# Kernel optimization log

Hardware: AMD Instinct MI355X
Metric: run time of the kernel (lower is better)

Reference implementation:

```python
import jax, jax.numpy as jnp
import numpy as np

BLOCK = 32          # MX block size (group_size)
E4M3_MAX = 448.0    # max finite value of float8_e4m3fn
E4M3_EMAX = 8       # max exponent of e4m3 (used for shared-exponent offset per MX spec)
TINY = 1e-38        # guard for log2(0)


def _quant_e4m3(v):
    """Fake-quantize v to the float8_e4m3fn grid with rint (round-half-even)."""
    a = jnp.abs(v)
    # exponent of each element, clamped to [min_normal_exp=-6, emax=8]
    e = jnp.clip(jnp.floor(jnp.log2(jnp.maximum(a, TINY))), -6.0, 8.0)
    step = jnp.exp2(e - 3.0)  # 3 mantissa bits
    q = jnp.clip(jnp.round(a / step) * step, 0.0, E4M3_MAX)
    return jnp.sign(v) * q


def mx_quant(v):
    """npu_dynamic_mx_quant(axis=-1, block_size=32, dst=e4m3, round=rint).
    Returns (q_blocks [..., K//32, 32], e8m0 scale [..., K//32])."""
    K = v.shape[-1]
    vb = v.reshape(*v.shape[:-1], K // BLOCK, BLOCK)
    amax = jnp.max(jnp.abs(vb), axis=-1)
    # shared exponent: floor(log2(amax)) - emax_elem, as an e8m0 power-of-two scale
    se = jnp.where(amax > 0,
                   jnp.floor(jnp.log2(jnp.maximum(amax, TINY))) - E4M3_EMAX,
                   0.0)
    scale = jnp.exp2(jnp.clip(se, -127.0, 127.0))
    q = _quant_e4m3(vb / scale[..., None])
    return q, scale


def setup_inputs() -> dict:
    key = jax.random.key(0)
    k1, k2, k3 = jax.random.split(key, 3)
    B, S, K, N = 2, 2048, 4096, 4096
    x = jax.random.normal(k1, (B, S, K), dtype=jnp.float32)
    weight = jax.random.normal(k2, (N, K), dtype=jnp.float32) * 0.02  # Linear weight [out, in]
    bias = jax.random.normal(k3, (N,), dtype=jnp.float32) * 0.01
    return {"x": x, "weight": weight, "bias": bias}


def reference(x, weight, bias):
    ori_shape = x.shape
    x2 = x.reshape(-1, ori_shape[-1])            # [M, K]
    # weight quantized once at init in the original module; same math here
    qw, sw = mx_quant(weight)                    # [N, K/32, 32], [N, K/32]
    qx, sx = mx_quant(x2)                        # [M, K/32, 32], [M, K/32]
    # group-scaled dequant-matmul: per-block scale product applied per group
    dqx = qx * sx[..., None]
    dqw = qw * sw[..., None]
    out = jnp.einsum('mgb,ngb->mn', dqx, dqw) + bias
    return out.reshape(*ori_shape[:-1], -1)
```

## Files before the change

kernel.cpp:

```cpp
#include <hip/hip_runtime.h>
#include <hip/hip_bf16.h>
#include <stdint.h>

typedef __attribute__((ext_vector_type(8)))  __bf16 bf16x8;
typedef __attribute__((ext_vector_type(16))) float  floatx16;
typedef unsigned short ushort8 __attribute__((ext_vector_type(8)));

__device__ __forceinline__ uint16_t f32_to_bf16_rn(float f) {
    uint32_t u = __float_as_uint(f);
    uint32_t r = u + 0x7FFFu + ((u >> 16) & 1u);
    return (uint16_t)(r >> 16);
}

__global__ __launch_bounds__(256) void quant_dq2_kernel(
    const float* __restrict__ x, const float* __restrict__ w,
    uint16_t* __restrict__ dqx, uint16_t* __restrict__ dqw,
    int nxh, int ntoth)
{
    int t = blockIdx.x * blockDim.x + threadIdx.x;
    if (t >= ntoth) return;
    const float* src; uint16_t* dst; int idx;
    if (t < nxh) { src = x; dst = dqx; idx = t; }
    else         { src = w; dst = dqw; idx = t - nxh; }

    const float4* p = (const float4*)src + (size_t)idx * 4;
    float4 v0 = p[0], v1 = p[1], v2 = p[2], v3 = p[3];
    float r[16] = {v0.x, v0.y, v0.z, v0.w, v1.x, v1.y, v1.z, v1.w,
                   v2.x, v2.y, v2.z, v2.w, v3.x, v3.y, v3.z, v3.w};

    float am = 0.0f;
#pragma unroll
    for (int i = 0; i < 16; ++i) am = fmaxf(am, fabsf(r[i]));
    am = fmaxf(am, __shfl_xor(am, 1));

    float scale, iscale;
    if (am > 0.0f) {
        int se = (int)((__float_as_uint(am) >> 23) & 0xFF) - 135;
        se = se < -127 ? -127 : se;
        scale  = __uint_as_float((uint32_t)(se + 127) << 23);
        iscale = __uint_as_float((uint32_t)(127 - se) << 23);
    } else {
        scale = 1.0f; iscale = 1.0f;
    }

    uint16_t o[16];
#pragma unroll
    for (int i = 0; i < 16; ++i) {
        float sv = r[i] * iscale;
        float a  = fabsf(sv);
        int e = (int)((__float_as_uint(a) >> 23) & 0xFF) - 127;
        e = e < -6 ? -6 : (e > 8 ? 8 : e);
        float step  = __uint_as_float((uint32_t)(e - 3 + 127) << 23);
        float rstep = __uint_as_float((uint32_t)(3 - e + 127) << 23);
        float q = rintf(a * rstep) * step;
        q = fminf(q, 448.0f);
        float dq = copysignf(q, sv) * scale;
        o[i] = f32_to_bf16_rn(dq);
    }
    ushort8 lo, hi;
#pragma unroll
    for (int i = 0; i < 8; ++i) { lo[i] = o[i]; hi[i] = o[i + 8]; }
    ((ushort8*)dst)[idx * 2]     = lo;
    ((ushort8*)dst)[idx * 2 + 1] = hi;
}

#define BM 128
#define BN 128
#define BK 64

__global__ __launch_bounds__(256) void gemm_bt_bias(
    const uint16_t* __restrict__ A, const uint16_t* __restrict__ B,
    const float* __restrict__ bias, float* __restrict__ C,
    int M, int N, int K)
{
    __shared__ uint16_t sA[BM * BK];
    __shared__ uint16_t sB[BN * BK];

    const int tid  = threadIdx.x;
    const int wave = tid >> 6;
    const int lane = tid & 63;

    const int bm = blockIdx.y * BM;
    const int bn = blockIdx.x * BN;

    const int srow8  = lane >> 3;
    const int schunk = (lane & 7) ^ srow8;
    const int wrow   = wave * 32;

    const uint16_t* Ag = A + (size_t)(bm + wrow + srow8) * K + schunk * 8;
    const uint16_t* Bg = B + (size_t)(bn + wrow + srow8) * K + schunk * 8;

    const int wm  = (wave & 1) * 64;
    const int wn  = (wave >> 1) * 64;
    const int m32 = lane & 31;
    const int h   = lane >> 5;
    const int swz = m32 & 7;

    floatx16 acc[2][2];
#pragma unroll
    for (int i = 0; i < 2; ++i)
#pragma unroll
        for (int j = 0; j < 2; ++j)
#pragma unroll
            for (int r = 0; r < 16; ++r) acc[i][j][r] = 0.0f;

    for (int k0 = 0; k0 < K; k0 += BK) {
        __syncthreads();
#pragma unroll
        for (int c = 0; c < 4; ++c) {
            __builtin_amdgcn_global_load_lds(
                (const __attribute__((address_space(1))) void*)(Ag + (size_t)c * 8 * K + k0),
                (__attribute__((address_space(3))) void*)(sA + (wrow + c * 8) * BK),
                16, 0, 0);
        }
#pragma unroll
        for (int c = 0; c < 4; ++c) {
            __builtin_amdgcn_global_load_lds(
                (const __attribute__((address_space(1))) void*)(Bg + (size_t)c * 8 * K + k0),
                (__attribute__((address_space(3))) void*)(sB + (wrow + c * 8) * BK),
                16, 0, 0);
        }
        __syncthreads();

#pragma unroll
        for (int kk = 0; kk < 4; ++kk) {
            const int chunk = kk * 2 + h;
            const int slot  = chunk ^ swz;
            bf16x8 a0 = *(const bf16x8*)(sA + (wm      + m32) * BK + slot * 8);
            bf16x8 a1 = *(const bf16x8*)(sA + (wm + 32 + m32) * BK + slot * 8);
            bf16x8 b0 = *(const bf16x8*)(sB + (wn      + m32) * BK + slot * 8);
            bf16x8 b1 = *(const bf16x8*)(sB + (wn + 32 + m32) * BK + slot * 8);
            acc[0][0] = __builtin_amdgcn_mfma_f32_32x32x16_bf16(a0, b0, acc[0][0], 0, 0, 0);
            acc[0][1] = __builtin_amdgcn_mfma_f32_32x32x16_bf16(a0, b1, acc[0][1], 0, 0, 0);
            acc[1][0] = __builtin_amdgcn_mfma_f32_32x32x16_bf16(a1, b0, acc[1][0], 0, 0, 0);
            acc[1][1] = __builtin_amdgcn_mfma_f32_32x32x16_bf16(a1, b1, acc[1][1], 0, 0, 0);
        }
    }

#pragma unroll
    for (int j = 0; j < 2; ++j) {
        const int col = bn + wn + j * 32 + m32;
        const float bz = bias[col];
#pragma unroll
        for (int i = 0; i < 2; ++i) {
            const int rbase = bm + wm + i * 32 + 4 * h;
#pragma unroll
            for (int r = 0; r < 16; ++r) {
                const int row = rbase + (r & 3) + 8 * (r >> 2);
                C[(size_t)row * N + col] = acc[i][j][r] + bz;
            }
        }
    }
}

extern "C" void kernel_launch(void* const* d_in, const int* in_sizes, int n_in,
                              void* d_out, int out_size, void* d_ws, size_t ws_size,
                              hipStream_t stream) {
    const float* x    = (const float*)d_in[0];
    const float* w    = (const float*)d_in[1];
    const float* bias = (const float*)d_in[2];
    float* out = (float*)d_out;

    const int N = in_sizes[2];
    const int K = in_sizes[1] / N;
    const int M = in_sizes[0] / K;

    uint16_t* dqx = (uint16_t*)d_ws;
    uint16_t* dqw = dqx + (size_t)M * K;

    const int nxh   = (M * K) / 16;
    const int ntoth = nxh + (N * K) / 16;
    quant_dq2_kernel<<<(ntoth + 255) / 256, 256, 0, stream>>>(x, w, dqx, dqw, nxh, ntoth);

    dim3 grid(N / BN, M / BM);
    gemm_bt_bias<<<grid, 256, 0, stream>>>(dqx, dqw, bias, out, M, N, K);
}
```

Before: 320.3 us.

## Use 256x256 tiles with double-buffered LDS pipeline and XCD-aware block remap

Enlarges the GEMM workgroup tile to 256x256 with 512 threads and moves operands into 128KB of dynamic LDS split into two buffers. The next K-tile is prefetched while MFMAs run on the current one, using vmcnt waits and raw barriers in place of __syncthreads. Block IDs are remapped across the 8 XCDs for L2 locality, and B fragments are preloaded in registers while s_setprio is raised around the MFMA groups. This aims to cut global-load stalls and raise arithmetic intensity, at the cost of more registers and LDS, which limits occupancy. The grid also shrinks to 256 workgroups on the 256-CU part, leaving no second wave of blocks to hide stalls.

```diff
diff --git a/kernel.cpp b/kernel.cpp
--- a/kernel.cpp
+++ b/kernel.cpp
@@ -64,90 +64,129 @@
     ((ushort8*)dst)[idx * 2 + 1] = hi;
 }
 
-#define BM 128
-#define BN 128
+#define BM 256
+#define BN 256
 #define BK 64
 
-__global__ __launch_bounds__(256) void gemm_bt_bias(
+__global__ __launch_bounds__(512, 2) void gemm_bt_bias(
     const uint16_t* __restrict__ A, const uint16_t* __restrict__ B,
     const float* __restrict__ bias, float* __restrict__ C,
     int M, int N, int K)
 {
-    __shared__ uint16_t sA[BM * BK];
-    __shared__ uint16_t sB[BN * BK];
+    extern __shared__ uint8_t lds[];
+    uint16_t* sA = (uint16_t*)lds;
+    uint16_t* sB = (uint16_t*)(lds + 65536);
 
     const int tid  = threadIdx.x;
     const int wave = tid >> 6;
     const int lane = tid & 63;
 
-    const int bm = blockIdx.y * BM;
-    const int bn = blockIdx.x * BN;
-
-    const int srow8  = lane >> 3;
-    const int schunk = (lane & 7) ^ srow8;
-    const int wrow   = wave * 32;
-
-    const uint16_t* Ag = A + (size_t)(bm + wrow + srow8) * K + schunk * 8;
-    const uint16_t* Bg = B + (size_t)(bn + wrow + srow8) * K + schunk * 8;
-
-    const int wm  = (wave & 1) * 64;
-    const int wn  = (wave >> 1) * 64;
+    int lin = blockIdx.y * gridDim.x + blockIdx.x;
+    const int nwg = gridDim.x * gridDim.y;
+    if ((nwg & 7) == 0) {
+        const int q = nwg >> 3;
+        lin = (lin & 7) * q + (lin >> 3);
+    }
+    const int bm = (lin / gridDim.x) * BM;
+    const int bn = (lin % gridDim.x) * BN;
+
+    const int srow   = tid >> 3;
+    const int schunk = ((tid & 7) ^ (srow & 7)) * 8;
+    const uint16_t* Ag = A + (size_t)(bm + srow) * K + schunk;
+    const uint16_t* Bg = B + (size_t)(bn + srow) * K + schunk;
+    const size_t c64K = (size_t)64 * K;
+    uint8_t* dA0 = lds + wave * 1024;
+    uint8_t* dB0 = lds + 65536 + wave * 1024;
+
+    const int wm  = (wave >> 2) * 128;
+    const int wn  = (wave & 3) * 64;
     const int m32 = lane & 31;
     const int h   = lane >> 5;
     const int swz = m32 & 7;
 
-    floatx16 acc[2][2];
-#pragma unroll
-    for (int i = 0; i < 2; ++i)
+    floatx16 acc[4][2];
+#pragma unroll
+    for (int i = 0; i < 4; ++i)
 #pragma unroll
         for (int j = 0; j < 2; ++j)
 #pragma unroll
             for (int r = 0; r < 16; ++r) acc[i][j][r] = 0.0f;
 
-    for (int k0 = 0; k0 < K; k0 += BK) {
-        __syncthreads();
-#pragma unroll
-        for (int c = 0; c < 4; ++c) {
+    auto stage = [&](int buf, int tk) {
+        const size_t k0 = (size_t)tk * BK;
+        uint8_t* dA = dA0 + buf * 32768;
+        uint8_t* dB = dB0 + buf * 32768;
+#pragma unroll
+        for (int c = 0; c < 4; ++c)
             __builtin_amdgcn_global_load_lds(
-                (const __attribute__((address_space(1))) void*)(Ag + (size_t)c * 8 * K + k0),
-                (__attribute__((address_space(3))) void*)(sA + (wrow + c * 8) * BK),
-                16, 0, 0);
-        }
-#pragma unroll
-        for (int c = 0; c < 4; ++c) {
+                (const __attribute__((address_space(1))) void*)(Ag + c * c64K + k0),
+                (__attribute__((address_space(3))) void*)(dA + c * 8192), 16, 0, 0);
+#pragma unroll
+        for (int c = 0; c < 4; ++c)
             __builtin_amdgcn_global_load_lds(
-                (const __attribute__((address_space(1))) void*)(Bg + (size_t)c * 8 * K + k0),
-                (__attribute__((address_space(3))) void*)(sB + (wrow + c * 8) * BK),
-                16, 0, 0);
-        }
-        __syncthreads();
-
-#pragma unroll
-        for (int kk = 0; kk < 4; ++kk) {
-            const int chunk = kk * 2 + h;
-            const int slot  = chunk ^ swz;
-            bf16x8 a0 = *(const bf16x8*)(sA + (wm      + m32) * BK + slot * 8);
-            bf16x8 a1 = *(const bf16x8*)(sA + (wm + 32 + m32) * BK + slot * 8);
-            bf16x8 b0 = *(const bf16x8*)(sB + (wn      + m32) * BK + slot * 8);
-            bf16x8 b1 = *(const bf16x8*)(sB + (wn + 32 + m32) * BK + slot * 8);
-            acc[0][0] = __builtin_amdgcn_mfma_f32_32x32x16_bf16(a0, b0, acc[0][0], 0, 0, 0);
-            acc[0][1] = __builtin_amdgcn_mfma_f32_32x32x16_bf16(a0, b1, acc[0][1], 0, 0, 0);
-            acc[1][0] = __builtin_amdgcn_mfma_f32_32x32x16_bf16(a1, b0, acc[1][0], 0, 0, 0);
-            acc[1][1] = __builtin_amdgcn_mfma_f32_32x32x16_bf16(a1, b1, acc[1][1], 0, 0, 0);
-        }
-    }
-
-#pragma unroll
-    for (int j = 0; j < 2; ++j) {
-        const int col = bn + wn + j * 32 + m32;
+                (const __attribute__((address_space(1))) void*)(Bg + c * c64K + k0),
+                (__attribute__((address_space(3))) void*)(dB + c * 8192), 16, 0, 0);
+    };
+
+    const int NT = K / BK;
+    stage(0, 0);
+
+    for (int t = 0; t < NT; ++t) {
+        const int cur = t & 1;
+        if (t + 1 < NT) {
+            stage(cur ^ 1, t + 1);
+            asm volatile("s_waitcnt vmcnt(8)" ::: "memory");
+        } else {
+            asm volatile("s_waitcnt vmcnt(0)" ::: "memory");
+        }
+        __builtin_amdgcn_s_barrier();
+        __builtin_amdgcn_sched_barrier(0);
+
+        const uint16_t* bufA = sA + cur * 16384;
+        const uint16_t* bufB = sB + cur * 16384;
+
+        bf16x8 bB[2][4];
+#pragma unroll
+        for (int nj = 0; nj < 2; ++nj) {
+            const int row = wn + nj * 32 + m32;
+#pragma unroll
+            for (int ks = 0; ks < 4; ++ks) {
+                const int slot = (ks * 2 + h) ^ swz;
+                bB[nj][ks] = *(const bf16x8*)(bufB + row * BK + slot * 8);
+            }
+        }
+#pragma unroll
+        for (int mi = 0; mi < 4; ++mi) {
+            const int row = wm + mi * 32 + m32;
+            bf16x8 aA[4];
+#pragma unroll
+            for (int ks = 0; ks < 4; ++ks) {
+                const int slot = (ks * 2 + h) ^ swz;
+                aA[ks] = *(const bf16x8*)(bufA + row * BK + slot * 8);
+            }
+            __builtin_amdgcn_s_setprio(1);
+#pragma unroll
+            for (int ks = 0; ks < 4; ++ks) {
+                acc[mi][0] = __builtin_amdgcn_mfma_f32_32x32x16_bf16(aA[ks], bB[0][ks], acc[mi][0], 0, 0, 0);
+                acc[mi][1] = __builtin_amdgcn_mfma_f32_32x32x16_bf16(aA[ks], bB[1][ks], acc[mi][1], 0, 0, 0);
+            }
+            __builtin_amdgcn_s_setprio(0);
+        }
+        __builtin_amdgcn_sched_barrier(0);
+        __builtin_amdgcn_s_barrier();
+    }
+
+#pragma unroll
+    for (int nj = 0; nj < 2; ++nj) {
+        const int col = bn + wn + nj * 32 + m32;
         const float bz = bias[col];
 #pragma unroll
-        for (int i = 0; i < 2; ++i) {
-            const int rbase = bm + wm + i * 32 + 4 * h;
+        for (int mi = 0; mi < 4; ++mi) {
+            const int rbase = bm + wm + mi * 32 + 4 * h;
 #pragma unroll
             for (int r = 0; r < 16; ++r) {
                 const int row = rbase + (r & 3) + 8 * (r >> 2);
-                C[(size_t)row * N + col] = acc[i][j][r] + bz;
+                C[(size_t)row * N + col] = acc[mi][nj][r] + bz;
             }
         }
     }
@@ -172,6 +211,8 @@
     const int ntoth = nxh + (N * K) / 16;
     quant_dq2_kernel<<<(ntoth + 255) / 256, 256, 0, stream>>>(x, w, dqx, dqw, nxh, ntoth);
 
+    hipFuncSetAttribute((const void*)gemm_bt_bias,
+                        hipFuncAttributeMaxDynamicSharedMemorySize, 131072);
     dim3 grid(N / BN, M / BM);
-    gemm_bt_bias<<<grid, 256, 0, stream>>>(dqx, dqw, bias, out, M, N, K);
-}
+    gemm_bt_bias<<<grid, 512, 131072, stream>>>(dqx, dqw, bias, out, M, N, K);
+}
```

Result: faster. 291.5 us (-9.0%).
